# Kernel optimization log

Hardware: AMD Instinct MI355X
Metric: run time of the kernel (lower is better)

## Reference

```python
import jax, jax.numpy as jnp
import numpy as np

GRID_SIZE = 5
SPLINE_ORDER = 3
B, D, O = 16384, 512, 512


def _make_grid():
    h = 2.0 / GRID_SIZE
    # matches torch.arange(-k, grid_size + k + 1) * h - 2.0  -> 12 knots
    return jnp.arange(-SPLINE_ORDER, GRID_SIZE + SPLINE_ORDER + 1, dtype=jnp.float32) * h - 2.0


def _bspline_basis(x, grid):
    # x: [B, D]; grid: [G] with G = grid_size + 2*order + 1 = 12
    G = grid.shape[0]
    xe = x[..., None]                      # [B, D, 1]
    g = grid.reshape(1, 1, G)              # [1, 1, G]
    # degree-0: indicator of knot interval  -> [B, D, G-1]
    bases = ((xe >= g[:, :, :-1]) & (xe < g[:, :, 1:])).astype(x.dtype)
    eps = 1e-9
    for k in range(1, SPLINE_ORDER + 1):   # Cox-de Boor recursion, width shrinks by 1 each step
        left = (xe - g[:, :, :-k - 1]) / (g[:, :, k:-1] - g[:, :, :-k - 1] + eps)
        right = (g[:, :, k + 1:] - xe) / (g[:, :, k + 1:] - g[:, :, 1:-k] + eps)
        bases = left * bases[..., :-1] + right * bases[..., 1:]
    return bases                           # [B, D, grid_size + order] = [B, D, 8]


def setup_inputs() -> dict:
    key = jax.random.key(0)
    k1, k2, k3 = jax.random.split(key, 3)
    x = jax.random.normal(k1, (B, D), dtype=jnp.float32)
    # kaiming_uniform_(a=sqrt(5)*0.1): bound = sqrt(6 / ((1 + a^2) * fan_in))
    a = np.sqrt(5.0) * 0.1
    bound = float(np.sqrt(6.0 / ((1.0 + a * a) * D)))
    base_weight = jax.random.uniform(k2, (O, D), dtype=jnp.float32, minval=-bound, maxval=bound)
    spline_weight = jax.random.normal(k3, (O, D, GRID_SIZE + SPLINE_ORDER), dtype=jnp.float32) * 0.01
    return {"x": x, "base_weight": base_weight, "spline_weight": spline_weight}


def reference(x, base_weight, spline_weight):
    grid = _make_grid()
    base_output = jnp.matmul(jax.nn.silu(x), base_weight.T)      # [B, O]
    x_norm = jnp.clip(x, -2.0, 2.0)
    basis = _bspline_basis(x_norm, grid)                          # [B, D, 8]
    spline_output = jnp.einsum('bic,oic->bo', basis, spline_weight)
    return base_output + spline_output
```

## Files before the change

### kernel.cpp

```cpp
#include <hip/hip_runtime.h>
#include <cstdint>
#include <cstddef>
#include <type_traits>

#define B_ROWS 16384
#define D_DIM  512
#define O_DIM  512
#define BM 64
#define BN 512
#define BK 32

typedef __bf16 bf16;
typedef __attribute__((ext_vector_type(8))) bf16  bf16x8;
typedef __attribute__((ext_vector_type(4))) float f32x4;

__device__ __forceinline__ uint32_t pk2(float a, float b) {
    uint16_t ua = __builtin_bit_cast(uint16_t, (__bf16)a);
    uint16_t ub = __builtin_bit_cast(uint16_t, (__bf16)b);
    return (uint32_t)ua | ((uint32_t)ub << 16);
}

__device__ __forceinline__ void spline_pairs(float xv, uint32_t out[4]) {
    float xn = fminf(fmaxf(xv, -2.0f), 2.0f);
    float t  = (xn + 3.2f) * 2.5f;
    int   j0 = (int)t;
    float u  = t - (float)j0;
    float u2 = u * u, u3 = u2 * u, omu = 1.0f - u;
    const float s6 = 1.0f / 6.0f;
    float w0 = omu * omu * omu * s6;
    float w1 = (3.0f * u3 - 6.0f * u2 + 4.0f) * s6;
    float w2 = (-3.0f * u3 + 3.0f * u2 + 3.0f * u + 1.0f) * s6;
    float w3 = u3 * s6;
    uint64_t W64 = ((uint64_t)pk2(w2, w3) << 32) | pk2(w0, w1);
    int sh = (j0 - 3) * 16;
    uint64_t lo = W64 << (sh & 63);
    uint64_t hi = W64 >> ((64 - sh) & 63);
    uint32_t lo_lo = (uint32_t)lo, lo_hi = (uint32_t)(lo >> 32);
    uint32_t hi_lo = (uint32_t)hi, hi_hi = (uint32_t)(hi >> 32);
    bool lt64 = sh < 64, eq0 = (sh == 0), lt128 = sh < 128;
    out[0] = lt64 ? lo_lo : 0u;
    out[1] = lt64 ? lo_hi : 0u;
    out[2] = lt64 ? (eq0 ? 0u : hi_lo) : (lt128 ? lo_lo : 0u);
    out[3] = lt64 ? (eq0 ? 0u : hi_hi) : (lt128 ? lo_hi : 0u);
}

__global__ void pack_w_kernel(const float* __restrict__ bw,
                              const float* __restrict__ sw,
                              bf16* __restrict__ W) {
    int idx = blockIdx.x * blockDim.x + threadIdx.x;
    if (idx >= O_DIM * 64) return;
    int o  = idx >> 6;
    int i0 = (idx & 63) * 8;

    bf16 ob[9][8];
    const float* bwp = bw + (size_t)o * D_DIM + i0;
#pragma unroll
    for (int e = 0; e < 8; e++) {
        ob[0][e] = (bf16)bwp[e];
        const float* sp = sw + ((size_t)o * D_DIM + i0 + e) * 8;
#pragma unroll
        for (int c = 0; c < 8; c++)
            ob[c + 1][e] = (bf16)sp[c];
    }
    const int c   = i0 >> 5;
    const int sub = (i0 & 31) >> 3;
    const int cb  = o >> 4;
    const int ln  = (o & 15) + sub * 16;
#pragma unroll
    for (int f = 0; f < 9; f++) {
        size_t off = ((size_t)((f * 16 + c) * 32 + cb) * 64 + ln) * 8;
        *(bf16x8*)(W + off) = *(const bf16x8*)ob[f];
    }
}

#define BARA asm volatile("s_waitcnt lgkmcnt(0)\n\ts_barrier" ::: "memory")

__global__ __launch_bounds__(512, 2)
void gemm_fused_kernel(const float* __restrict__ x, const bf16* __restrict__ Wf,
                       float* __restrict__ C) {
    __shared__ __align__(16) bf16 As0[BM * BK], As1[BM * BK], As2[BM * BK], As3[BM * BK];

    const int tid  = threadIdx.x;
    const int bid  = blockIdx.x;
    const int m0   = bid * BM;
    const int wave = tid >> 6;
    const int lane = tid & 63;
    const int wn   = wave * 64;
    const int l15  = lane & 15;
    const int quad = lane >> 4;
    const int swz  = (l15 >> 1) & 3;
    const int aoff = l15 * BK + (quad ^ swz) * 8;

    const int rA = tid >> 3;
    const int q4 = tid & 7;
    const float* xrow = x + (size_t)(m0 + rA) * D_DIM + q4 * 4;
    const int awo = rA * BK + (((q4 >> 1) ^ ((rA >> 1) & 3)) * 8) + (q4 & 1) * 4;

    const bf16* gBf = Wf + ((size_t)((wn >> 4) * 64 + lane)) * 8;

    bf16* const AsArr[4] = {As0, As1, As2, As3};

    f32x4 acc[4][4] = {};
    bf16x8 brA[4], brB[4];
    uint32_t vpk[2][4][4];
    float xe[4];

    auto write_pack = [&](bf16* slab, const uint32_t (&P)[4][4], int j) {
        const int pr = j >> 1;
        uint32_t o[2];
#pragma unroll
        for (int m = 0; m < 2; m++) {
            uint32_t lo = P[pr][2*m], hi = P[pr][2*m+1];
            o[m] = (j & 1) ? ((lo >> 16) | (hi & 0xFFFF0000u))
                           : ((lo & 0xFFFFu) | (hi << 16));
        }
        *(uint2*)(slab + awo) = *(const uint2*)o;
    };
    auto write_silu = [&](bf16* slab) {
        float sl[4];
#pragma unroll
        for (int e = 0; e < 4; e++)
            sl[e] = xe[e] * __builtin_amdgcn_rcpf(1.0f + __expf(-xe[e]));
        uint32_t o[2] = {pk2(sl[0],sl[1]), pk2(sl[2],sl[3])};
        *(uint2*)(slab + awo) = *(const uint2*)o;
    };

    {
#pragma unroll
        for (int jn = 0; jn < 4; jn++)
            brA[jn] = *(const bf16x8*)(gBf + jn * 512);
        float4 a = *(const float4*)xrow;
        xe[0]=a.x; xe[1]=a.y; xe[2]=a.z; xe[3]=a.w;
#pragma unroll
        for (int e = 0; e < 4; e++) {
            uint32_t o4[4];
            spline_pairs(xe[e], o4);
            vpk[0][0][e]=o4[0]; vpk[0][1][e]=o4[1];
            vpk[0][2][e]=o4[2]; vpk[0][3][e]=o4[3];
        }
        write_silu(As0);
        write_pack(As1, vpk[0], 0);
        BARA;
    }

    auto step_body = [&](auto c4v, auto fv, int c) {
        constexpr int C4 = decltype(c4v)::value;
        constexpr int F  = decltype(fv)::value;
        constexpr int PC = C4 & 1;
        constexpr int TP = (C4 + F) & 1;
        constexpr int AR = (C4 + F) & 3;
        constexpr int AW = (C4 + F + 2) & 3;

        if (F == 0 && c < 15) {
            float4 a = *(const float4*)(xrow + (c + 1) * 32);
            xe[0]=a.x; xe[1]=a.y; xe[2]=a.z; xe[3]=a.w;
        }
        if (!(c == 15 && F == 8)) {
            const int tN = (F < 8) ? ((F + 1) * 16 + c) : (c + 1);
            const bf16* src = gBf + (size_t)tN * 16384;
            if constexpr (TP == 0) {
#pragma unroll
                for (int jn = 0; jn < 4; jn++)
                    brB[jn] = *(const bf16x8*)(src + jn * 512);
            } else {
#pragma unroll
                for (int jn = 0; jn < 4; jn++)
                    brA[jn] = *(const bf16x8*)(src + jn * 512);
            }
        }
        bf16x8 af[4];
#pragma unroll
        for (int tt = 0; tt < 4; tt++)
            af[tt] = *(const bf16x8*)(AsArr[AR] + tt * 16 * BK + aoff);

        if constexpr (F >= 1 && F <= 4) {
            if (c < 15) {
                uint32_t o4[4];
                spline_pairs(xe[F - 1], o4);
                vpk[PC ^ 1][0][F-1]=o4[0]; vpk[PC ^ 1][1][F-1]=o4[1];
                vpk[PC ^ 1][2][F-1]=o4[2]; vpk[PC ^ 1][3][F-1]=o4[3];
            }
        }
        if constexpr (F <= 6) {
            write_pack(AsArr[AW], vpk[PC], F + 1);
        } else if constexpr (F == 7) {
            if (c < 15) write_silu(AsArr[AW]);
        } else {
            if (c < 15) write_pack(AsArr[AW], vpk[PC ^ 1], 0);
        }

        __builtin_amdgcn_s_setprio(1);
#pragma unroll
        for (int im = 0; im < 4; im++)
#pragma unroll
            for (int jn = 0; jn < 4; jn++)
                acc[im][jn] = __builtin_amdgcn_mfma_f32_16x16x32_bf16(
                    af[im], (TP == 0) ? brA[jn] : brB[jn], acc[im][jn], 0, 0, 0);
        __builtin_amdgcn_s_setprio(0);

        if constexpr (TP == 1) {
            if (!(c == 15 && F == 8)) BARA;
        }
    };

#define IC(n) std::integral_constant<int,(n)>{}
    auto chunk_body = [&](auto c4v, int c) {
        step_body(c4v, IC(0), c); step_body(c4v, IC(1), c); step_body(c4v, IC(2), c);
        step_body(c4v, IC(3), c); step_body(c4v, IC(4), c); step_body(c4v, IC(5), c);
        step_body(c4v, IC(6), c); step_body(c4v, IC(7), c); step_body(c4v, IC(8), c);
    };

    for (int cc = 0; cc < 16; cc += 4) {
        chunk_body(IC(0), cc);
        chunk_body(IC(1), cc + 1);
        chunk_body(IC(2), cc + 2);
        chunk_body(IC(3), cc + 3);
    }
#undef IC

#pragma unroll
    for (int im = 0; im < 4; im++) {
        const int rbase = m0 + im * 16 + quad * 4;
#pragma unroll
        for (int jn = 0; jn < 4; jn++) {
            const int col = wn + jn * 16 + l15;
#pragma unroll
            for (int rr = 0; rr < 4; rr++)
                C[(size_t)(rbase + rr) * O_DIM + col] = acc[im][jn][rr];
        }
    }
}

extern "C" void kernel_launch(void* const* d_in, const int* in_sizes, int n_in,
                              void* d_out, int out_size, void* d_ws, size_t ws_size,
                              hipStream_t stream) {
    const float* x  = (const float*)d_in[0];
    const float* bw = (const float*)d_in[1];
    const float* sw = (const float*)d_in[2];
    float* out = (float*)d_out;

    const size_t Wbytes = (size_t)144 * 32 * 64 * 8 * sizeof(bf16);
    if (ws_size < Wbytes) return;
    bf16* W = (bf16*)d_ws;

    pack_w_kernel<<<(O_DIM * 64 + 255) / 256, 256, 0, stream>>>(bw, sw, W);
    gemm_fused_kernel<<<dim3(B_ROWS / BM), dim3(512), 0, stream>>>(x, W, out);
}
```

Before: 152.8 us.

## Deepen LDS ring to eight slabs and triple-buffer B fragments

Expands the shared-memory A-slab ring from four to eight buffers so a barrier is needed only every four steps instead of every two. A fragments for two consecutive steps are loaded together. B fragments are triple-buffered so each global load runs two steps ahead. The aim is to cut barrier count and hide global load latency better. The cost is double the LDS and more registers, which may reduce occupancy under the 512-thread, 2-block launch bounds.

```diff
diff --git a/kernel.cpp b/kernel.cpp
--- a/kernel.cpp
+++ b/kernel.cpp
@@ -79,6 +79,7 @@
 void gemm_fused_kernel(const float* __restrict__ x, const bf16* __restrict__ Wf,
                        float* __restrict__ C) {
     __shared__ __align__(16) bf16 As0[BM * BK], As1[BM * BK], As2[BM * BK], As3[BM * BK];
+    __shared__ __align__(16) bf16 As4[BM * BK], As5[BM * BK], As6[BM * BK], As7[BM * BK];
 
     const int tid  = threadIdx.x;
     const int bid  = blockIdx.x;
@@ -98,13 +99,20 @@
 
     const bf16* gBf = Wf + ((size_t)((wn >> 4) * 64 + lane)) * 8;
 
-    bf16* const AsArr[4] = {As0, As1, As2, As3};
+    bf16* const AsArr[8] = {As0, As1, As2, As3, As4, As5, As6, As7};
 
     f32x4 acc[4][4] = {};
-    bf16x8 brA[4], brB[4];
+    bf16x8 br0[4], br1[4], br2[4];
+    bf16x8 afE[4], afO[4];
     uint32_t vpk[2][4][4];
     float xe[4];
 
+    auto loadB = [&](bf16x8 (&dst)[4], int tIdx) {
+        const bf16* src = gBf + (size_t)tIdx * 16384;
+#pragma unroll
+        for (int jn = 0; jn < 4; jn++)
+            dst[jn] = *(const bf16x8*)(src + jn * 512);
+    };
     auto write_pack = [&](bf16* slab, const uint32_t (&P)[4][4], int j) {
         const int pr = j >> 1;
         uint32_t o[2];
@@ -124,11 +132,20 @@
         uint32_t o[2] = {pk2(sl[0],sl[1]), pk2(sl[2],sl[3])};
         *(uint2*)(slab + awo) = *(const uint2*)o;
     };
+    auto domfma = [&](bf16x8 (&a)[4], bf16x8 (&b)[4]) {
+        __builtin_amdgcn_s_setprio(1);
+#pragma unroll
+        for (int im = 0; im < 4; im++)
+#pragma unroll
+            for (int jn = 0; jn < 4; jn++)
+                acc[im][jn] = __builtin_amdgcn_mfma_f32_16x16x32_bf16(
+                    a[im], b[jn], acc[im][jn], 0, 0, 0);
+        __builtin_amdgcn_s_setprio(0);
+    };
 
     {
-#pragma unroll
-        for (int jn = 0; jn < 4; jn++)
-            brA[jn] = *(const bf16x8*)(gBf + jn * 512);
+        loadB(br0, 0);
+        loadB(br1, 16);
         float4 a = *(const float4*)xrow;
         xe[0]=a.x; xe[1]=a.y; xe[2]=a.z; xe[3]=a.w;
 #pragma unroll
@@ -140,39 +157,42 @@
         }
         write_silu(As0);
         write_pack(As1, vpk[0], 0);
+        write_pack(As2, vpk[0], 1);
+        write_pack(As3, vpk[0], 2);
         BARA;
     }
 
-    auto step_body = [&](auto c4v, auto fv, int c) {
-        constexpr int C4 = decltype(c4v)::value;
-        constexpr int F  = decltype(fv)::value;
-        constexpr int PC = C4 & 1;
-        constexpr int TP = (C4 + F) & 1;
-        constexpr int AR = (C4 + F) & 3;
-        constexpr int AW = (C4 + F + 2) & 3;
+    auto step_body = [&](auto c8v, auto fv, int c) {
+        constexpr int C8  = decltype(c8v)::value;
+        constexpr int F   = decltype(fv)::value;
+        constexpr int PC  = C8 & 1;
+        constexpr int TP  = (C8 + F) & 1;
+        constexpr int ARE = (C8 + F) & 7;
+        constexpr int ARO = (C8 + F + 1) & 7;
+        constexpr int AW  = (C8 + F + 4) & 7;
+        constexpr int BR  = F % 3;
+        constexpr int BW  = (F + 2) % 3;
 
         if (F == 0 && c < 15) {
             float4 a = *(const float4*)(xrow + (c + 1) * 32);
             xe[0]=a.x; xe[1]=a.y; xe[2]=a.z; xe[3]=a.w;
         }
-        if (!(c == 15 && F == 8)) {
-            const int tN = (F < 8) ? ((F + 1) * 16 + c) : (c + 1);
-            const bf16* src = gBf + (size_t)tN * 16384;
-            if constexpr (TP == 0) {
-#pragma unroll
-                for (int jn = 0; jn < 4; jn++)
-                    brB[jn] = *(const bf16x8*)(src + jn * 512);
-            } else {
-#pragma unroll
-                for (int jn = 0; jn < 4; jn++)
-                    brA[jn] = *(const bf16x8*)(src + jn * 512);
-            }
-        }
-        bf16x8 af[4];
-#pragma unroll
-        for (int tt = 0; tt < 4; tt++)
-            af[tt] = *(const bf16x8*)(AsArr[AR] + tt * 16 * BK + aoff);
-
+        if (!(c == 15 && F >= 7)) {
+            const int tN = (F <= 6) ? ((F + 2) * 16 + c)
+                         : (F == 7) ? (c + 1)
+                                    : (16 + c + 1);
+            if constexpr (BW == 0)      loadB(br0, tN);
+            else if constexpr (BW == 1) loadB(br1, tN);
+            else                        loadB(br2, tN);
+        }
+        if constexpr (TP == 0) {
+#pragma unroll
+            for (int tt = 0; tt < 4; tt++)
+                afE[tt] = *(const bf16x8*)(AsArr[ARE] + tt * 16 * BK + aoff);
+#pragma unroll
+            for (int tt = 0; tt < 4; tt++)
+                afO[tt] = *(const bf16x8*)(AsArr[ARO] + tt * 16 * BK + aoff);
+        }
         if constexpr (F >= 1 && F <= 4) {
             if (c < 15) {
                 uint32_t o4[4];
@@ -181,40 +201,45 @@
                 vpk[PC ^ 1][2][F-1]=o4[2]; vpk[PC ^ 1][3][F-1]=o4[3];
             }
         }
-        if constexpr (F <= 6) {
-            write_pack(AsArr[AW], vpk[PC], F + 1);
-        } else if constexpr (F == 7) {
+        if constexpr (F <= 4) {
+            write_pack(AsArr[AW], vpk[PC], F + 3);
+        } else if constexpr (F == 5) {
             if (c < 15) write_silu(AsArr[AW]);
         } else {
-            if (c < 15) write_pack(AsArr[AW], vpk[PC ^ 1], 0);
-        }
-
-        __builtin_amdgcn_s_setprio(1);
-#pragma unroll
-        for (int im = 0; im < 4; im++)
-#pragma unroll
-            for (int jn = 0; jn < 4; jn++)
-                acc[im][jn] = __builtin_amdgcn_mfma_f32_16x16x32_bf16(
-                    af[im], (TP == 0) ? brA[jn] : brB[jn], acc[im][jn], 0, 0, 0);
-        __builtin_amdgcn_s_setprio(0);
-
-        if constexpr (TP == 1) {
+            if (c < 15) write_pack(AsArr[AW], vpk[PC ^ 1], F - 6);
+        }
+
+        if constexpr (TP == 0) {
+            if constexpr (BR == 0)      domfma(afE, br0);
+            else if constexpr (BR == 1) domfma(afE, br1);
+            else                        domfma(afE, br2);
+        } else {
+            if constexpr (BR == 0)      domfma(afO, br0);
+            else if constexpr (BR == 1) domfma(afO, br1);
+            else                        domfma(afO, br2);
+        }
+
+        if constexpr (((C8 + F) & 3) == 3) {
             if (!(c == 15 && F == 8)) BARA;
         }
     };
 
 #define IC(n) std::integral_constant<int,(n)>{}
-    auto chunk_body = [&](auto c4v, int c) {
-        step_body(c4v, IC(0), c); step_body(c4v, IC(1), c); step_body(c4v, IC(2), c);
-        step_body(c4v, IC(3), c); step_body(c4v, IC(4), c); step_body(c4v, IC(5), c);
-        step_body(c4v, IC(6), c); step_body(c4v, IC(7), c); step_body(c4v, IC(8), c);
-    };
-
-    for (int cc = 0; cc < 16; cc += 4) {
+    auto chunk_body = [&](auto c8v, int c) {
+        step_body(c8v, IC(0), c); step_body(c8v, IC(1), c); step_body(c8v, IC(2), c);
+        step_body(c8v, IC(3), c); step_body(c8v, IC(4), c); step_body(c8v, IC(5), c);
+        step_body(c8v, IC(6), c); step_body(c8v, IC(7), c); step_body(c8v, IC(8), c);
+    };
+
+    for (int cc = 0; cc < 16; cc += 8) {
         chunk_body(IC(0), cc);
         chunk_body(IC(1), cc + 1);
         chunk_body(IC(2), cc + 2);
         chunk_body(IC(3), cc + 3);
+        chunk_body(IC(4), cc + 4);
+        chunk_body(IC(5), cc + 5);
+        chunk_body(IC(6), cc + 6);
+        chunk_body(IC(7), cc + 7);
     }
 #undef IC
 
```

Result: no change. 154.6 us (+1.2%).

## Double threads per block to 1024, halving per-wave N tile and A loads

Applied to the files above, without the earlier changes.

Launches 1024 threads (16 waves) per block instead of 512, so each wave covers 32 output columns rather than 64 and each thread loads and spline-expands 2 x values instead of 4. This cuts per-thread register pressure and spline work, aiming for more waves in flight to hide latency. The cost is fewer MFMAs per A-fragment load, so the LDS-read-to-compute ratio doubles, and more waves contend at each barrier.

```diff
diff --git a/kernel.cpp b/kernel.cpp
--- a/kernel.cpp
+++ b/kernel.cpp
@@ -75,7 +75,7 @@
 
 #define BARA asm volatile("s_waitcnt lgkmcnt(0)\n\ts_barrier" ::: "memory")
 
-__global__ __launch_bounds__(512, 2)
+__global__ __launch_bounds__(1024, 4)
 void gemm_fused_kernel(const float* __restrict__ x, const bf16* __restrict__ Wf,
                        float* __restrict__ C) {
     __shared__ __align__(16) bf16 As0[BM * BK], As1[BM * BK], As2[BM * BK], As3[BM * BK];
@@ -85,54 +85,61 @@
     const int m0   = bid * BM;
     const int wave = tid >> 6;
     const int lane = tid & 63;
-    const int wn   = wave * 64;
+    const int wn   = wave * 32;
     const int l15  = lane & 15;
     const int quad = lane >> 4;
     const int swz  = (l15 >> 1) & 3;
     const int aoff = l15 * BK + (quad ^ swz) * 8;
 
-    const int rA = tid >> 3;
-    const int q4 = tid & 7;
-    const float* xrow = x + (size_t)(m0 + rA) * D_DIM + q4 * 4;
-    const int awo = rA * BK + (((q4 >> 1) ^ ((rA >> 1) & 3)) * 8) + (q4 & 1) * 4;
+    const int rA = tid >> 4;
+    const int q2 = tid & 15;
+    const float* xrow = x + (size_t)(m0 + rA) * D_DIM + q2 * 2;
+    const int awo = rA * BK + (((q2 >> 2) ^ ((rA >> 1) & 3)) * 8) + (q2 & 3) * 2;
 
     const bf16* gBf = Wf + ((size_t)((wn >> 4) * 64 + lane)) * 8;
 
     bf16* const AsArr[4] = {As0, As1, As2, As3};
 
-    f32x4 acc[4][4] = {};
-    bf16x8 brA[4], brB[4];
-    uint32_t vpk[2][4][4];
-    float xe[4];
-
-    auto write_pack = [&](bf16* slab, const uint32_t (&P)[4][4], int j) {
+    f32x4 acc[4][2] = {};
+    bf16x8 brA[2], brB[2];
+    uint32_t vpk[2][4][2];
+    float xe[2];
+
+    auto loadB = [&](bf16x8 (&dst)[2], int tIdx) {
+        const bf16* src = gBf + (size_t)tIdx * 16384;
+#pragma unroll
+        for (int jn = 0; jn < 2; jn++)
+            dst[jn] = *(const bf16x8*)(src + jn * 512);
+    };
+    auto write_pack = [&](bf16* slab, const uint32_t (&P)[4][2], int j) {
         const int pr = j >> 1;
-        uint32_t o[2];
-#pragma unroll
-        for (int m = 0; m < 2; m++) {
-            uint32_t lo = P[pr][2*m], hi = P[pr][2*m+1];
-            o[m] = (j & 1) ? ((lo >> 16) | (hi & 0xFFFF0000u))
-                           : ((lo & 0xFFFFu) | (hi << 16));
-        }
-        *(uint2*)(slab + awo) = *(const uint2*)o;
+        uint32_t lo = P[pr][0], hi = P[pr][1];
+        uint32_t o = (j & 1) ? ((lo >> 16) | (hi & 0xFFFF0000u))
+                             : ((lo & 0xFFFFu) | (hi << 16));
+        *(uint32_t*)(slab + awo) = o;
     };
     auto write_silu = [&](bf16* slab) {
-        float sl[4];
-#pragma unroll
-        for (int e = 0; e < 4; e++)
-            sl[e] = xe[e] * __builtin_amdgcn_rcpf(1.0f + __expf(-xe[e]));
-        uint32_t o[2] = {pk2(sl[0],sl[1]), pk2(sl[2],sl[3])};
-        *(uint2*)(slab + awo) = *(const uint2*)o;
+        float s0 = xe[0] * __builtin_amdgcn_rcpf(1.0f + __expf(-xe[0]));
+        float s1 = xe[1] * __builtin_amdgcn_rcpf(1.0f + __expf(-xe[1]));
+        *(uint32_t*)(slab + awo) = pk2(s0, s1);
+    };
+    auto domfma = [&](bf16x8 (&a)[4], bf16x8 (&b)[2]) {
+        __builtin_amdgcn_s_setprio(1);
+#pragma unroll
+        for (int im = 0; im < 4; im++)
+#pragma unroll
+            for (int jn = 0; jn < 2; jn++)
+                acc[im][jn] = __builtin_amdgcn_mfma_f32_16x16x32_bf16(
+                    a[im], b[jn], acc[im][jn], 0, 0, 0);
+        __builtin_amdgcn_s_setprio(0);
     };
 
     {
-#pragma unroll
-        for (int jn = 0; jn < 4; jn++)
-            brA[jn] = *(const bf16x8*)(gBf + jn * 512);
-        float4 a = *(const float4*)xrow;
-        xe[0]=a.x; xe[1]=a.y; xe[2]=a.z; xe[3]=a.w;
-#pragma unroll
-        for (int e = 0; e < 4; e++) {
+        loadB(brA, 0);
+        float2 a = *(const float2*)xrow;
+        xe[0] = a.x; xe[1] = a.y;
+#pragma unroll
+        for (int e = 0; e < 2; e++) {
             uint32_t o4[4];
             spline_pairs(xe[e], o4);
             vpk[0][0][e]=o4[0]; vpk[0][1][e]=o4[1];
@@ -152,28 +159,20 @@
         constexpr int AW = (C4 + F + 2) & 3;
 
         if (F == 0 && c < 15) {
-            float4 a = *(const float4*)(xrow + (c + 1) * 32);
-            xe[0]=a.x; xe[1]=a.y; xe[2]=a.z; xe[3]=a.w;
+            float2 a = *(const float2*)(xrow + (c + 1) * 32);
+            xe[0] = a.x; xe[1] = a.y;
         }
         if (!(c == 15 && F == 8)) {
             const int tN = (F < 8) ? ((F + 1) * 16 + c) : (c + 1);
-            const bf16* src = gBf + (size_t)tN * 16384;
-            if constexpr (TP == 0) {
-#pragma unroll
-                for (int jn = 0; jn < 4; jn++)
-                    brB[jn] = *(const bf16x8*)(src + jn * 512);
-            } else {
-#pragma unroll
-                for (int jn = 0; jn < 4; jn++)
-                    brA[jn] = *(const bf16x8*)(src + jn * 512);
-            }
+            if constexpr (TP == 0) loadB(brB, tN);
+            else                   loadB(brA, tN);
         }
         bf16x8 af[4];
 #pragma unroll
         for (int tt = 0; tt < 4; tt++)
             af[tt] = *(const bf16x8*)(AsArr[AR] + tt * 16 * BK + aoff);
 
-        if constexpr (F >= 1 && F <= 4) {
+        if constexpr (F >= 1 && F <= 2) {
             if (c < 15) {
                 uint32_t o4[4];
                 spline_pairs(xe[F - 1], o4);
@@ -189,14 +188,8 @@
             if (c < 15) write_pack(AsArr[AW], vpk[PC ^ 1], 0);
         }
 
-        __builtin_amdgcn_s_setprio(1);
-#pragma unroll
-        for (int im = 0; im < 4; im++)
-#pragma unroll
-            for (int jn = 0; jn < 4; jn++)
-                acc[im][jn] = __builtin_amdgcn_mfma_f32_16x16x32_bf16(
-                    af[im], (TP == 0) ? brA[jn] : brB[jn], acc[im][jn], 0, 0, 0);
-        __builtin_amdgcn_s_setprio(0);
+        if constexpr (TP == 0) domfma(af, brA);
+        else                   domfma(af, brB);
 
         if constexpr (TP == 1) {
             if (!(c == 15 && F == 8)) BARA;
@@ -222,7 +215,7 @@
     for (int im = 0; im < 4; im++) {
         const int rbase = m0 + im * 16 + quad * 4;
 #pragma unroll
-        for (int jn = 0; jn < 4; jn++) {
+        for (int jn = 0; jn < 2; jn++) {
             const int col = wn + jn * 16 + l15;
 #pragma unroll
             for (int rr = 0; rr < 4; rr++)
@@ -244,5 +237,5 @@
     bf16* W = (bf16*)d_ws;
 
     pack_w_kernel<<<(O_DIM * 64 + 255) / 256, 256, 0, stream>>>(bw, sw, W);
-    gemm_fused_kernel<<<dim3(B_ROWS / BM), dim3(512), 0, stream>>>(x, W, out);
-}
+    gemm_fused_kernel<<<dim3(B_ROWS / BM), dim3(1024), 0, stream>>>(x, W, out);
+}
```

Result: no change. 154.8 us (+1.3%).
